# Kernel tuning notes

Measured on AMD Instinct MI355X. Metric: run time of the kernel, lower is better.

Reference implementation:

```python
import jax, jax.numpy as jnp
import numpy as np

N_NODES = 100000


def gcn_conv(x, W, b, src, dst, n):
    """PyG GCNConv: add self-loops, symmetric normalization, aggregate."""
    x = x @ W  # [N, out]
    loop = jnp.arange(n, dtype=src.dtype)
    src_f = jnp.concatenate([src, loop])  # sources (message origins)
    dst_f = jnp.concatenate([dst, loop])  # targets (aggregation index)
    ones = jnp.ones(src_f.shape[0], dtype=x.dtype)
    deg = jax.ops.segment_sum(ones, dst_f, num_segments=n)
    dinv = jnp.where(deg > 0, jax.lax.rsqrt(deg), 0.0)
    norm = dinv[src_f] * dinv[dst_f]  # [E+N]
    msg = x[src_f] * norm[:, None]  # gather + scale
    out = jax.ops.segment_sum(msg, dst_f, num_segments=n)  # scatter-add
    return out + b


def setup_inputs() -> dict:
    key = jax.random.key(0)
    k1, k2, k3, k4 = jax.random.split(key, 4)
    in_f, hid, ncls = 128, 128, 64
    n_edges = 1600000
    x = jax.random.normal(k1, (N_NODES, in_f), dtype=jnp.float32)
    W1 = jax.random.normal(k2, (in_f, hid), dtype=jnp.float32) * (1.0 / np.sqrt(in_f))
    b1 = jnp.zeros((hid,), dtype=jnp.float32)
    W2 = jax.random.normal(k3, (hid, ncls), dtype=jnp.float32) * (1.0 / np.sqrt(hid))
    b2 = jnp.zeros((ncls,), dtype=jnp.float32)
    edge_index = jax.random.randint(k4, (2, n_edges), 0, N_NODES, dtype=jnp.int32)
    return {"x": x, "W1": W1, "b1": b1, "W2": W2, "b2": b2, "edge_index": edge_index}


def reference(x, W1, b1, W2, b2, edge_index):
    src, dst = edge_index[0], edge_index[1]
    n = x.shape[0]
    h = gcn_conv(x, W1, b1, src, dst, n)
    h = jax.nn.relu(h)
    # dropout p=0.5 is identity in eval mode
    h = gcn_conv(h, W2, b2, src, dst, n)
    return jax.nn.log_softmax(h, axis=1)
```

## Files before the change

### kernel.cpp

```cpp
#include <hip/hip_runtime.h>
#include <math.h>

#define N_NODES 100000
#define N_EDGES 1600000
#define NB 391
#define MROWS 100096
#define CH 3200
#define ZROW N_NODES

typedef __attribute__((ext_vector_type(8))) short short8;
typedef __attribute__((ext_vector_type(4))) float f32x4;
typedef __attribute__((ext_vector_type(2))) float f32x2;

__device__ __forceinline__ short f2b(float f) {
    unsigned u = __float_as_uint(f);
    unsigned r = (u + 0x7FFFu + ((u >> 16) & 1u)) >> 16;
    return (short)r;
}
__device__ __forceinline__ unsigned pk2(float a, float b) {
    return (unsigned)(unsigned short)f2b(a) | ((unsigned)(unsigned short)f2b(b) << 16);
}
__device__ __forceinline__ unsigned char f2q(float v) {
    return (unsigned char)(__builtin_amdgcn_cvt_pk_fp8_f32(v, 0.f, 0, false) & 0xFF);
}
__device__ __forceinline__ void acc2(f32x2* a, unsigned u) {
    a[0] += __builtin_amdgcn_cvt_pk_f32_fp8((int)u, false);
    a[1] += __builtin_amdgcn_cvt_pk_f32_fp8((int)u, true);
}

__device__ __forceinline__ short8 pack8t(const float* __restrict__ p) {
    float4 v0 = ((const float4*)p)[0];
    float4 v1 = ((const float4*)p)[1];
    union { unsigned u[4]; short8 s; } r;
    r.u[0] = __builtin_amdgcn_perm(__float_as_uint(v0.y), __float_as_uint(v0.x), 0x07060302u);
    r.u[1] = __builtin_amdgcn_perm(__float_as_uint(v0.w), __float_as_uint(v0.z), 0x07060302u);
    r.u[2] = __builtin_amdgcn_perm(__float_as_uint(v1.y), __float_as_uint(v1.x), 0x07060302u);
    r.u[3] = __builtin_amdgcn_perm(__float_as_uint(v1.w), __float_as_uint(v1.z), 0x07060302u);
    return r.s;
}

__global__ __launch_bounds__(512) void init_misc(int* __restrict__ bcnt,
                                                 unsigned* __restrict__ y1s,
                                                 unsigned* __restrict__ y2s) {
    int t = threadIdx.x;
    if (t < NB) bcnt[t] = 0;
    if (t < 32) y1s[t] = 0;
    if (t < 16) y2s[t] = 0;
}

__global__ __launch_bounds__(256) void bucket_count(const int* __restrict__ dst,
                                                    int* __restrict__ bcnt) {
    __shared__ int h[NB];
    int t = threadIdx.x;
    for (int i = t; i < NB; i += 256) h[i] = 0;
    __syncthreads();
    for (int e = blockIdx.x * 256 + t; e < N_EDGES; e += gridDim.x * 256)
        atomicAdd(&h[dst[e] >> 8], 1);
    __syncthreads();
    for (int i = t; i < NB; i += 256)
        if (h[i]) atomicAdd(&bcnt[i], h[i]);
}

__global__ __launch_bounds__(512) void bucket_scan(const int* __restrict__ bcnt,
                                                   int* __restrict__ boffs,
                                                   int* __restrict__ bcur) {
    __shared__ int s[512];
    int t = threadIdx.x;
    int v = (t < NB) ? bcnt[t] : 0;
    s[t] = v;
    __syncthreads();
    for (int off = 1; off < 512; off <<= 1) {
        int u = (t >= off) ? s[t - off] : 0;
        __syncthreads();
        s[t] += u;
        __syncthreads();
    }
    if (t < NB) {
        int ex = s[t] - v;
        boffs[t] = ex;
        bcur[t] = ex;
    }
    if (t == 0) boffs[NB] = N_EDGES;
}

__global__ __launch_bounds__(256) void bucket_scatter(const int* __restrict__ src,
                                                      const int* __restrict__ dst,
                                                      int* __restrict__ bcur,
                                                      unsigned* __restrict__ pairs) {
    __shared__ unsigned lw[CH];
    __shared__ short lb[CH];
    __shared__ int cnt[NB];
    __shared__ int lstart[NB];
    int t = threadIdx.x;
    int e0 = blockIdx.x * CH;
    int n = min(CH, N_EDGES - e0);
    for (int i = t; i < NB; i += 256) cnt[i] = 0;
    __syncthreads();
    for (int i = t; i < n; i += 256) {
        int s = src[e0 + i], d = dst[e0 + i];
        lw[i] = ((unsigned)(d & 255) << 24) | (unsigned)s;
        int b = d >> 8;
        lb[i] = (short)b;
        atomicAdd(&cnt[b], 1);
    }
    __syncthreads();
    for (int b = t; b < NB; b += 256) {
        int c = cnt[b];
        lstart[b] = c ? atomicAdd(&bcur[b], c) : 0;
        cnt[b] = 0;
    }
    __syncthreads();
    for (int i = t; i < n; i += 256) {
        int b = lb[i];
        int lo = atomicAdd(&cnt[b], 1);
        pairs[lstart[b] + lo] = lw[i];
    }
}

__global__ __launch_bounds__(256) void csr_fill_bucket(const unsigned* __restrict__ pairs,
                                                       const int* __restrict__ boffs,
                                                       int2* __restrict__ rinfo,
                                                       float* __restrict__ dinv,
                                                       int* __restrict__ srcs) {
    __shared__ int lcnt[256];
    __shared__ int ls[256];
    int t = threadIdx.x, b = blockIdx.x, base = b << 8;
    lcnt[t] = 0;
    __syncthreads();
    int lo_e = boffs[b], hi_e = boffs[b + 1];
    for (int i = lo_e + t; i < hi_e; i += 256)
        atomicAdd(&lcnt[pairs[i] >> 24], 1);
    __syncthreads();
    int c = lcnt[t];
    int cpad = (c + 8) & ~7;
    ls[t] = cpad;
    __syncthreads();
    for (int off = 1; off < 256; off <<= 1) {
        int u = (t >= off) ? ls[t - off] : 0;
        __syncthreads();
        ls[t] += u;
        __syncthreads();
    }
    int pbase = ((lo_e + 7) & ~7) + b * 2056;
    int rp = pbase + ls[t] - cpad;
    int node = base + t;
    if (node < N_NODES) {
        rinfo[node] = make_int2(rp, rp + cpad);
        dinv[node] = rsqrtf((float)(c + 1));
        srcs[rp] = node;
    }
    __syncthreads();
    lcnt[t] = rp + 1;
    __syncthreads();
    for (int i = lo_e + t; i < hi_e; i += 256) {
        unsigned p = pairs[i];
        int li = p >> 24;
        int pos = atomicAdd(&lcnt[li], 1);
        srcs[pos] = (int)(p & 0xFFFFFFu);
    }
    __syncthreads();
    for (int i = lcnt[t], stop = rp + cpad; i < stop; ++i) srcs[i] = ZROW;
}

__global__ __launch_bounds__(256) void convert_w(const float* __restrict__ W1,
                                                 const float* __restrict__ W2,
                                                 short* __restrict__ w1h,
                                                 short* __restrict__ w2h) {
    int id = blockIdx.x * 256 + threadIdx.x;
    if (id < 128 * 128) {
        int n = id >> 7, k = id & 127;
        w1h[id] = f2b(W1[k * 128 + n]);
    } else if (id < 128 * 128 + 64 * 128) {
        int j = id - 128 * 128;
        int n = j >> 7, k = j & 127;
        w2h[j] = f2b(W2[k * 64 + n]);
    }
}

__global__ __launch_bounds__(512) void gemm1_mfma(const float* __restrict__ X,
                                                  const short* __restrict__ Wt,
                                                  const float* __restrict__ dinv,
                                                  unsigned char* __restrict__ Yf) {
    __shared__ short Ws[128 * 128];
    const int t = threadIdx.x;
    for (int i = t * 8; i < 128 * 128; i += 512 * 8)
        *(short8*)(Ws + i) = *(const short8*)(Wt + i);
    __syncthreads();

    const int w = t >> 6, lane = t & 63;
    const int m = lane & 15, q = lane >> 4;
    const int r0 = blockIdx.x * 128 + w * 16;
    const int ra = min(r0 + m, N_NODES - 1);

    f32x4 acc[8];
#pragma unroll
    for (int c = 0; c < 8; ++c) acc[c] = (f32x4)(0.f);

#pragma unroll
    for (int kk = 0; kk < 4; ++kk) {
        const int koff = kk * 32 + q * 8;
        short8 a = pack8t(X + (size_t)ra * 128 + koff);
#pragma unroll
        for (int c = 0; c < 8; ++c) {
            short8 bh = *(const short8*)(Ws + (c * 16 + m) * 128 + koff);
            acc[c] = __builtin_amdgcn_mfma_f32_16x16x32_bf16(a, bh, acc[c], 0, 0, 0);
        }
    }

    const int rb0 = r0 + q * 4;
    f32x4 dv = *(const f32x4*)(dinv + rb0);
#pragma unroll
    for (int c = 0; c < 8; ++c) {
        const int col = c * 16 + m;
#pragma unroll
        for (int r = 0; r < 4; ++r) {
            int row = rb0 + r;
            if (row < N_NODES) Yf[(size_t)row * 128 + col] = f2q(acc[c][r] * dv[r]);
        }
    }
}

__global__ __launch_bounds__(512) void gemm2_mfma(const short* __restrict__ H,
                                                  const short* __restrict__ Wt,
                                                  const float* __restrict__ dinv,
                                                  unsigned char* __restrict__ Yf) {
    __shared__ short Ws[64 * 128];
    const int t = threadIdx.x;
    for (int i = t * 8; i < 64 * 128; i += 512 * 8)
        *(short8*)(Ws + i) = *(const short8*)(Wt + i);
    __syncthreads();

    const int w = t >> 6, lane = t & 63;
    const int m = lane & 15, q = lane >> 4;
    const int r0 = blockIdx.x * 128 + w * 16;

    f32x4 acc[4];
#pragma unroll
    for (int c = 0; c < 4; ++c) acc[c] = (f32x4)(0.f);

#pragma unroll
    for (int kk = 0; kk < 4; ++kk) {
        const int koff = kk * 32 + q * 8;
        short8 a = *(const short8*)(H + (size_t)(r0 + m) * 128 + koff);
#pragma unroll
        for (int c = 0; c < 4; ++c) {
            short8 bh = *(const short8*)(Ws + (c * 16 + m) * 128 + koff);
            acc[c] = __builtin_amdgcn_mfma_f32_16x16x32_bf16(a, bh, acc[c], 0, 0, 0);
        }
    }

    const int rb0 = r0 + q * 4;
    f32x4 dv = *(const f32x4*)(dinv + rb0);
#pragma unroll
    for (int c = 0; c < 4; ++c) {
        const int col = c * 16 + m;
#pragma unroll
        for (int r = 0; r < 4; ++r) {
            int row = rb0 + r;
            if (row < N_NODES) Yf[(size_t)row * 64 + col] = f2q(acc[c][r] * dv[r]);
        }
    }
}

__global__ __launch_bounds__(256) void agg_relu(const int2* __restrict__ rinfo,
                                                const int* __restrict__ srcs,
                                                const unsigned char* __restrict__ Yf,
                                                const float* __restrict__ dinv,
                                                const float* __restrict__ b,
                                                short* __restrict__ Hb) {
    int t = threadIdx.x;
    int lane = t & 63, w = t >> 6;
    int half = lane >> 5, li = lane & 31;
    int d0 = blockIdx.x * 8 + 2 * w;
    int d1 = d0 + 1;
    const unsigned fo = (unsigned)(li << 2);
    int2 r0 = rinfo[d0], r1 = rinfo[d1];
    f32x2 a0[2] = {(f32x2)(0.f), (f32x2)(0.f)};
    f32x2 a1[2] = {(f32x2)(0.f), (f32x2)(0.f)};
    int e0 = r0.x, n0 = r0.y, e1 = r1.x, n1 = r1.y;
    uint4 s0 = *(const uint4*)(srcs + e0 + 4 * half);
    uint4 s1 = *(const uint4*)(srcs + e1 + 4 * half);
    bool c0 = true, c1 = true;
    for (;;) {
        bool p0 = c0, p1 = c1;
        unsigned g00, g01, g02, g03, g10, g11, g12, g13;
        if (p0) {
            g00 = *(const unsigned*)(Yf + (((unsigned)s0.x << 7) + fo));
            g01 = *(const unsigned*)(Yf + (((unsigned)s0.y << 7) + fo));
            g02 = *(const unsigned*)(Yf + (((unsigned)s0.z << 7) + fo));
            g03 = *(const unsigned*)(Yf + (((unsigned)s0.w << 7) + fo));
            e0 += 8;
            c0 = e0 < n0;
        }
        if (p1) {
            g10 = *(const unsigned*)(Yf + (((unsigned)s1.x << 7) + fo));
            g11 = *(const unsigned*)(Yf + (((unsigned)s1.y << 7) + fo));
            g12 = *(const unsigned*)(Yf + (((unsigned)s1.z << 7) + fo));
            g13 = *(const unsigned*)(Yf + (((unsigned)s1.w << 7) + fo));
            e1 += 8;
            c1 = e1 < n1;
        }
        if (c0) s0 = *(const uint4*)(srcs + e0 + 4 * half);
        if (c1) s1 = *(const uint4*)(srcs + e1 + 4 * half);
        if (p0) { acc2(a0, g00); acc2(a0, g01); acc2(a0, g02); acc2(a0, g03); }
        if (p1) { acc2(a1, g10); acc2(a1, g11); acc2(a1, g12); acc2(a1, g13); }
        if (!(c0 | c1)) break;
    }
    float t00 = a0[0][0], t01 = a0[0][1], t02 = a0[1][0], t03 = a0[1][1];
    float t10 = a1[0][0], t11 = a1[0][1], t12 = a1[1][0], t13 = a1[1][1];
    t00 += __shfl_xor(t00, 32); t01 += __shfl_xor(t01, 32);
    t02 += __shfl_xor(t02, 32); t03 += __shfl_xor(t03, 32);
    t10 += __shfl_xor(t10, 32); t11 += __shfl_xor(t11, 32);
    t12 += __shfl_xor(t12, 32); t13 += __shfl_xor(t13, 32);
    int dd = half ? d1 : d0;
    float s0f = half ? t10 : t00;
    float s1f = half ? t11 : t01;
    float s2f = half ? t12 : t02;
    float s3f = half ? t13 : t03;
    float sc = dinv[dd];
    float4 bb = ((const float4*)b)[li];
    float v0 = fmaxf(sc * s0f + bb.x, 0.f);
    float v1 = fmaxf(sc * s1f + bb.y, 0.f);
    float v2 = fmaxf(sc * s2f + bb.z, 0.f);
    float v3 = fmaxf(sc * s3f + bb.w, 0.f);
    ((uint2*)Hb)[(size_t)dd * 32 + li] = make_uint2(pk2(v0, v1), pk2(v2, v3));
}

__global__ __launch_bounds__(256) void agg_lsm(const int2* __restrict__ rinfo,
                                               const int* __restrict__ srcs,
                                               const unsigned char* __restrict__ Yf,
                                               const float* __restrict__ dinv,
                                               const float* __restrict__ b,
                                               float* __restrict__ out) {
    int t = threadIdx.x;
    int lane = t & 63, w = t >> 6;
    int gi = lane >> 4, li = lane & 15;
    int d0 = blockIdx.x * 8 + 2 * w;
    int d1 = d0 + 1;
    const unsigned fo = (unsigned)(li << 2);
    int2 r0 = rinfo[d0], r1 = rinfo[d1];
    f32x2 a0[2] = {(f32x2)(0.f), (f32x2)(0.f)};
    f32x2 a1[2] = {(f32x2)(0.f), (f32x2)(0.f)};
    int e0 = r0.x, n0 = r0.y, e1 = r1.x, n1 = r1.y;
    uint2 s0 = *(const uint2*)(srcs + e0 + 2 * gi);
    uint2 s1 = *(const uint2*)(srcs + e1 + 2 * gi);
    bool c0 = true, c1 = true;
    for (;;) {
        bool p0 = c0, p1 = c1;
        unsigned g00, g01, g10, g11;
        if (p0) {
            g00 = *(const unsigned*)(Yf + (((unsigned)s0.x << 6) + fo));
            g01 = *(const unsigned*)(Yf + (((unsigned)s0.y << 6) + fo));
            e0 += 8;
            c0 = e0 < n0;
        }
        if (p1) {
            g10 = *(const unsigned*)(Yf + (((unsigned)s1.x << 6) + fo));
            g11 = *(const unsigned*)(Yf + (((unsigned)s1.y << 6) + fo));
            e1 += 8;
            c1 = e1 < n1;
        }
        if (c0) s0 = *(const uint2*)(srcs + e0 + 2 * gi);
        if (c1) s1 = *(const uint2*)(srcs + e1 + 2 * gi);
        if (p0) { acc2(a0, g00); acc2(a0, g01); }
        if (p1) { acc2(a1, g10); acc2(a1, g11); }
        if (!(c0 | c1)) break;
    }
    float t00 = a0[0][0], t01 = a0[0][1], t02 = a0[1][0], t03 = a0[1][1];
    float t10 = a1[0][0], t11 = a1[0][1], t12 = a1[1][0], t13 = a1[1][1];
    t00 += __shfl_xor(t00, 16); t00 += __shfl_xor(t00, 32);
    t01 += __shfl_xor(t01, 16); t01 += __shfl_xor(t01, 32);
    t02 += __shfl_xor(t02, 16); t02 += __shfl_xor(t02, 32);
    t03 += __shfl_xor(t03, 16); t03 += __shfl_xor(t03, 32);
    t10 += __shfl_xor(t10, 16); t10 += __shfl_xor(t10, 32);
    t11 += __shfl_xor(t11, 16); t11 += __shfl_xor(t11, 32);
    t12 += __shfl_xor(t12, 16); t12 += __shfl_xor(t12, 32);
    t13 += __shfl_xor(t13, 16); t13 += __shfl_xor(t13, 32);
    int gsel = gi >> 1;
    int dd = gsel ? d1 : d0;
    float s0f = gsel ? t10 : t00;
    float s1f = gsel ? t11 : t01;
    float s2f = gsel ? t12 : t02;
    float s3f = gsel ? t13 : t03;
    float sc = dinv[dd];
    float4 bb = ((const float4*)b)[li];
    float v0 = sc * s0f + bb.x;
    float v1 = sc * s1f + bb.y;
    float v2 = sc * s2f + bb.z;
    float v3 = sc * s3f + bb.w;
    float m = fmaxf(fmaxf(v0, v1), fmaxf(v2, v3));
#pragma unroll
    for (int o = 1; o <= 8; o <<= 1) m = fmaxf(m, __shfl_xor(m, o));
    float su = __expf(v0 - m) + __expf(v1 - m) + __expf(v2 - m) + __expf(v3 - m);
#pragma unroll
    for (int o = 1; o <= 8; o <<= 1) su += __shfl_xor(su, o);
    float ls = m + logf(su);
    if ((gi & 1) == 0)
        ((float4*)out)[(size_t)dd * 16 + li] =
            make_float4(v0 - ls, v1 - ls, v2 - ls, v3 - ls);
}

extern "C" void kernel_launch(void* const* d_in, const int* in_sizes, int n_in,
                              void* d_out, int out_size, void* d_ws, size_t ws_size,
                              hipStream_t stream) {
    const float* x  = (const float*)d_in[0];
    const float* W1 = (const float*)d_in[1];
    const float* b1 = (const float*)d_in[2];
    const float* W2 = (const float*)d_in[3];
    const float* b2 = (const float*)d_in[4];
    const int* edge = (const int*)d_in[5];
    const int* src = edge;
    const int* dst = edge + N_EDGES;
    float* out = (float*)d_out;

    char* ws = (char*)d_ws;
    int*           bcnt  = (int*)(ws + 0);
    int*           boffs = (int*)(ws + 2048);
    int*           bcur  = (int*)(ws + 4096);
    float*         dinv  = (float*)(ws + 6144);
    int2*          rinfo = (int2*)(ws + 406528);
    int*           srcs  = (int*)(ws + 1206528);
    unsigned*      pairs = (unsigned*)(ws + 14012672);
    short*         w1h   = (short*)(ws + 20412672);
    short*         w2h   = (short*)(ws + 20445440);
    unsigned char* y1f   = (unsigned char*)(ws + 20461824);
    short*         h1b   = (short*)(ws + 33274112);
    unsigned char* y2f   = (unsigned char*)(ws + 58898688);

    init_misc<<<1, 512, 0, stream>>>(bcnt,
                                     (unsigned*)(y1f + (size_t)N_NODES * 128),
                                     (unsigned*)(y2f + (size_t)N_NODES * 64));

    bucket_count<<<512, 256, 0, stream>>>(dst, bcnt);
    bucket_scan<<<1, 512, 0, stream>>>(bcnt, boffs, bcur);
    bucket_scatter<<<(N_EDGES + CH - 1) / CH, 256, 0, stream>>>(src, dst, bcur, pairs);
    csr_fill_bucket<<<NB, 256, 0, stream>>>(pairs, boffs, rinfo, dinv, srcs);

    convert_w<<<(128 * 128 + 64 * 128 + 255) / 256, 256, 0, stream>>>(W1, W2, w1h, w2h);

    gemm1_mfma<<<MROWS / 128, 512, 0, stream>>>(x, w1h, dinv, y1f);
    agg_relu<<<N_NODES / 8, 256, 0, stream>>>(rinfo, srcs, y1f, dinv, b1, h1b);

    gemm2_mfma<<<MROWS / 128, 512, 0, stream>>>(h1b, w2h, dinv, y2f);
    agg_lsm<<<N_NODES / 8, 256, 0, stream>>>(rinfo, srcs, y2f, dinv, b2, out);
}
```

Measured before the change: 262.8 us.

## Remap aggregation kernels to small lane groups per node with 16-byte gathers

Both aggregation kernels now give each destination node a small group of lanes: 8 lanes with 16 features each for layer 1, 4 lanes for layer 2. Each lane gathers 16-byte fp8 rows and software-pipelines the source-index and feature loads two steps ahead. This removes the cross-half shuffle reductions and uses wider loads, so each wave handles 8 or 16 nodes instead of 2. In exchange, each wave loops up to its longest node's degree, and the shorter nodes pad with loads from the zero row, which can waste bandwidth when degrees vary.

```diff
diff --git a/kernel.cpp b/kernel.cpp
--- a/kernel.cpp
+++ b/kernel.cpp
@@ -26,6 +26,9 @@
 __device__ __forceinline__ void acc2(f32x2* a, unsigned u) {
     a[0] += __builtin_amdgcn_cvt_pk_f32_fp8((int)u, false);
     a[1] += __builtin_amdgcn_cvt_pk_f32_fp8((int)u, true);
+}
+__device__ __forceinline__ void acc16(f32x2* a, uint4 u) {
+    acc2(a + 0, u.x); acc2(a + 2, u.y); acc2(a + 4, u.z); acc2(a + 6, u.w);
 }
 
 __device__ __forceinline__ short8 pack8t(const float* __restrict__ p) {
@@ -270,60 +273,52 @@
                                                 short* __restrict__ Hb) {
     int t = threadIdx.x;
     int lane = t & 63, w = t >> 6;
-    int half = lane >> 5, li = lane & 31;
-    int d0 = blockIdx.x * 8 + 2 * w;
-    int d1 = d0 + 1;
-    const unsigned fo = (unsigned)(li << 2);
-    int2 r0 = rinfo[d0], r1 = rinfo[d1];
-    f32x2 a0[2] = {(f32x2)(0.f), (f32x2)(0.f)};
-    f32x2 a1[2] = {(f32x2)(0.f), (f32x2)(0.f)};
-    int e0 = r0.x, n0 = r0.y, e1 = r1.x, n1 = r1.y;
-    uint4 s0 = *(const uint4*)(srcs + e0 + 4 * half);
-    uint4 s1 = *(const uint4*)(srcs + e1 + 4 * half);
-    bool c0 = true, c1 = true;
-    for (;;) {
-        bool p0 = c0, p1 = c1;
-        unsigned g00, g01, g02, g03, g10, g11, g12, g13;
-        if (p0) {
-            g00 = *(const unsigned*)(Yf + (((unsigned)s0.x << 7) + fo));
-            g01 = *(const unsigned*)(Yf + (((unsigned)s0.y << 7) + fo));
-            g02 = *(const unsigned*)(Yf + (((unsigned)s0.z << 7) + fo));
-            g03 = *(const unsigned*)(Yf + (((unsigned)s0.w << 7) + fo));
-            e0 += 8;
-            c0 = e0 < n0;
-        }
-        if (p1) {
-            g10 = *(const unsigned*)(Yf + (((unsigned)s1.x << 7) + fo));
-            g11 = *(const unsigned*)(Yf + (((unsigned)s1.y << 7) + fo));
-            g12 = *(const unsigned*)(Yf + (((unsigned)s1.z << 7) + fo));
-            g13 = *(const unsigned*)(Yf + (((unsigned)s1.w << 7) + fo));
-            e1 += 8;
-            c1 = e1 < n1;
-        }
-        if (c0) s0 = *(const uint4*)(srcs + e0 + 4 * half);
-        if (c1) s1 = *(const uint4*)(srcs + e1 + 4 * half);
-        if (p0) { acc2(a0, g00); acc2(a0, g01); acc2(a0, g02); acc2(a0, g03); }
-        if (p1) { acc2(a1, g10); acc2(a1, g11); acc2(a1, g12); acc2(a1, g13); }
-        if (!(c0 | c1)) break;
-    }
-    float t00 = a0[0][0], t01 = a0[0][1], t02 = a0[1][0], t03 = a0[1][1];
-    float t10 = a1[0][0], t11 = a1[0][1], t12 = a1[1][0], t13 = a1[1][1];
-    t00 += __shfl_xor(t00, 32); t01 += __shfl_xor(t01, 32);
-    t02 += __shfl_xor(t02, 32); t03 += __shfl_xor(t03, 32);
-    t10 += __shfl_xor(t10, 32); t11 += __shfl_xor(t11, 32);
-    t12 += __shfl_xor(t12, 32); t13 += __shfl_xor(t13, 32);
-    int dd = half ? d1 : d0;
-    float s0f = half ? t10 : t00;
-    float s1f = half ? t11 : t01;
-    float s2f = half ? t12 : t02;
-    float s3f = half ? t13 : t03;
-    float sc = dinv[dd];
-    float4 bb = ((const float4*)b)[li];
-    float v0 = fmaxf(sc * s0f + bb.x, 0.f);
-    float v1 = fmaxf(sc * s1f + bb.y, 0.f);
-    float v2 = fmaxf(sc * s2f + bb.z, 0.f);
-    float v3 = fmaxf(sc * s3f + bb.w, 0.f);
-    ((uint2*)Hb)[(size_t)dd * 32 + li] = make_uint2(pk2(v0, v1), pk2(v2, v3));
+    int g = lane >> 3, fl = lane & 7;
+    int node = blockIdx.x * 32 + w * 8 + g;
+    const unsigned fo = (unsigned)(fl << 4);
+    int2 r = rinfo[node];
+    int e = r.x, len = r.y - r.x;
+    int mx = len;
+    mx = max(mx, __shfl_xor(mx, 8));
+    mx = max(mx, __shfl_xor(mx, 16));
+    mx = max(mx, __shfl_xor(mx, 32));
+    f32x2 a[8];
+#pragma unroll
+    for (int i = 0; i < 8; ++i) a[i] = (f32x2)(0.f);
+
+    auto lsrc = [&](int i) -> unsigned {
+        int s = srcs[e + min(i, len - 1)];
+        return (i < len) ? (unsigned)s : (unsigned)ZROW;
+    };
+    unsigned sA0 = lsrc(0), sA1 = lsrc(1);
+    uint4 GA0 = *(const uint4*)(Yf + ((sA0 << 7) + fo));
+    uint4 GA1 = *(const uint4*)(Yf + ((sA1 << 7) + fo));
+    unsigned sB0 = lsrc(2), sB1 = lsrc(3);
+    for (int i = 0; i < mx; i += 2) {
+        uint4 GB0 = *(const uint4*)(Yf + ((sB0 << 7) + fo));
+        uint4 GB1 = *(const uint4*)(Yf + ((sB1 << 7) + fo));
+        unsigned sC0 = lsrc(i + 4), sC1 = lsrc(i + 5);
+        acc16(a, GA0); acc16(a, GA1);
+        GA0 = GB0; GA1 = GB1; sB0 = sC0; sB1 = sC1;
+    }
+
+    float sc = dinv[node];
+    const float4* bf = (const float4*)b;
+    float bb[16];
+    *(float4*)(bb + 0)  = bf[fl * 4 + 0];
+    *(float4*)(bb + 4)  = bf[fl * 4 + 1];
+    *(float4*)(bb + 8)  = bf[fl * 4 + 2];
+    *(float4*)(bb + 12) = bf[fl * 4 + 3];
+    unsigned u[8];
+#pragma unroll
+    for (int k = 0; k < 8; ++k) {
+        float v0 = fmaxf(sc * a[k][0] + bb[2 * k], 0.f);
+        float v1 = fmaxf(sc * a[k][1] + bb[2 * k + 1], 0.f);
+        u[k] = pk2(v0, v1);
+    }
+    uint4* hp = (uint4*)Hb + (size_t)node * 16 + fl * 2;
+    hp[0] = make_uint4(u[0], u[1], u[2], u[3]);
+    hp[1] = make_uint4(u[4], u[5], u[6], u[7]);
 }
 
 __global__ __launch_bounds__(256) void agg_lsm(const int2* __restrict__ rinfo,
@@ -334,70 +329,65 @@
                                                float* __restrict__ out) {
     int t = threadIdx.x;
     int lane = t & 63, w = t >> 6;
-    int gi = lane >> 4, li = lane & 15;
-    int d0 = blockIdx.x * 8 + 2 * w;
-    int d1 = d0 + 1;
-    const unsigned fo = (unsigned)(li << 2);
-    int2 r0 = rinfo[d0], r1 = rinfo[d1];
-    f32x2 a0[2] = {(f32x2)(0.f), (f32x2)(0.f)};
-    f32x2 a1[2] = {(f32x2)(0.f), (f32x2)(0.f)};
-    int e0 = r0.x, n0 = r0.y, e1 = r1.x, n1 = r1.y;
-    uint2 s0 = *(const uint2*)(srcs + e0 + 2 * gi);
-    uint2 s1 = *(const uint2*)(srcs + e1 + 2 * gi);
-    bool c0 = true, c1 = true;
-    for (;;) {
-        bool p0 = c0, p1 = c1;
-        unsigned g00, g01, g10, g11;
-        if (p0) {
-            g00 = *(const unsigned*)(Yf + (((unsigned)s0.x << 6) + fo));
-            g01 = *(const unsigned*)(Yf + (((unsigned)s0.y << 6) + fo));
-            e0 += 8;
-            c0 = e0 < n0;
-        }
-        if (p1) {
-            g10 = *(const unsigned*)(Yf + (((unsigned)s1.x << 6) + fo));
-            g11 = *(const unsigned*)(Yf + (((unsigned)s1.y << 6) + fo));
-            e1 += 8;
-            c1 = e1 < n1;
-        }
-        if (c0) s0 = *(const uint2*)(srcs + e0 + 2 * gi);
-        if (c1) s1 = *(const uint2*)(srcs + e1 + 2 * gi);
-        if (p0) { acc2(a0, g00); acc2(a0, g01); }
-        if (p1) { acc2(a1, g10); acc2(a1, g11); }
-        if (!(c0 | c1)) break;
-    }
-    float t00 = a0[0][0], t01 = a0[0][1], t02 = a0[1][0], t03 = a0[1][1];
-    float t10 = a1[0][0], t11 = a1[0][1], t12 = a1[1][0], t13 = a1[1][1];
-    t00 += __shfl_xor(t00, 16); t00 += __shfl_xor(t00, 32);
-    t01 += __shfl_xor(t01, 16); t01 += __shfl_xor(t01, 32);
-    t02 += __shfl_xor(t02, 16); t02 += __shfl_xor(t02, 32);
-    t03 += __shfl_xor(t03, 16); t03 += __shfl_xor(t03, 32);
-    t10 += __shfl_xor(t10, 16); t10 += __shfl_xor(t10, 32);
-    t11 += __shfl_xor(t11, 16); t11 += __shfl_xor(t11, 32);
-    t12 += __shfl_xor(t12, 16); t12 += __shfl_xor(t12, 32);
-    t13 += __shfl_xor(t13, 16); t13 += __shfl_xor(t13, 32);
-    int gsel = gi >> 1;
-    int dd = gsel ? d1 : d0;
-    float s0f = gsel ? t10 : t00;
-    float s1f = gsel ? t11 : t01;
-    float s2f = gsel ? t12 : t02;
-    float s3f = gsel ? t13 : t03;
-    float sc = dinv[dd];
-    float4 bb = ((const float4*)b)[li];
-    float v0 = sc * s0f + bb.x;
-    float v1 = sc * s1f + bb.y;
-    float v2 = sc * s2f + bb.z;
-    float v3 = sc * s3f + bb.w;
-    float m = fmaxf(fmaxf(v0, v1), fmaxf(v2, v3));
-#pragma unroll
-    for (int o = 1; o <= 8; o <<= 1) m = fmaxf(m, __shfl_xor(m, o));
-    float su = __expf(v0 - m) + __expf(v1 - m) + __expf(v2 - m) + __expf(v3 - m);
-#pragma unroll
-    for (int o = 1; o <= 8; o <<= 1) su += __shfl_xor(su, o);
+    int g = lane >> 2, fl = lane & 3;
+    int node = blockIdx.x * 64 + w * 16 + g;
+    int nd = min(node, N_NODES - 1);
+    const unsigned fo = (unsigned)(fl << 4);
+    int2 r = rinfo[nd];
+    int e = r.x, len = r.y - r.x;
+    int mx = len;
+    mx = max(mx, __shfl_xor(mx, 4));
+    mx = max(mx, __shfl_xor(mx, 8));
+    mx = max(mx, __shfl_xor(mx, 16));
+    mx = max(mx, __shfl_xor(mx, 32));
+    f32x2 a[8];
+#pragma unroll
+    for (int i = 0; i < 8; ++i) a[i] = (f32x2)(0.f);
+
+    auto lsrc = [&](int i) -> unsigned {
+        int s = srcs[e + min(i, len - 1)];
+        return (i < len) ? (unsigned)s : (unsigned)ZROW;
+    };
+    unsigned sA0 = lsrc(0), sA1 = lsrc(1);
+    uint4 GA0 = *(const uint4*)(Yf + ((sA0 << 6) + fo));
+    uint4 GA1 = *(const uint4*)(Yf + ((sA1 << 6) + fo));
+    unsigned sB0 = lsrc(2), sB1 = lsrc(3);
+    for (int i = 0; i < mx; i += 2) {
+        uint4 GB0 = *(const uint4*)(Yf + ((sB0 << 6) + fo));
+        uint4 GB1 = *(const uint4*)(Yf + ((sB1 << 6) + fo));
+        unsigned sC0 = lsrc(i + 4), sC1 = lsrc(i + 5);
+        acc16(a, GA0); acc16(a, GA1);
+        GA0 = GB0; GA1 = GB1; sB0 = sC0; sB1 = sC1;
+    }
+
+    float sc = dinv[nd];
+    const float4* bf = (const float4*)b;
+    float bb[16];
+    *(float4*)(bb + 0)  = bf[fl * 4 + 0];
+    *(float4*)(bb + 4)  = bf[fl * 4 + 1];
+    *(float4*)(bb + 8)  = bf[fl * 4 + 2];
+    *(float4*)(bb + 12) = bf[fl * 4 + 3];
+    float v[16];
+#pragma unroll
+    for (int j = 0; j < 16; ++j) v[j] = sc * a[j >> 1][j & 1] + bb[j];
+    float m = v[0];
+#pragma unroll
+    for (int j = 1; j < 16; ++j) m = fmaxf(m, v[j]);
+    m = fmaxf(m, __shfl_xor(m, 1));
+    m = fmaxf(m, __shfl_xor(m, 2));
+    float su = 0.f;
+#pragma unroll
+    for (int j = 0; j < 16; ++j) su += __expf(v[j] - m);
+    su += __shfl_xor(su, 1);
+    su += __shfl_xor(su, 2);
     float ls = m + logf(su);
-    if ((gi & 1) == 0)
-        ((float4*)out)[(size_t)dd * 16 + li] =
-            make_float4(v0 - ls, v1 - ls, v2 - ls, v3 - ls);
+    if (node < N_NODES) {
+        float4* op = (float4*)out + (size_t)node * 16 + fl * 4;
+        op[0] = make_float4(v[0] - ls,  v[1] - ls,  v[2] - ls,  v[3] - ls);
+        op[1] = make_float4(v[4] - ls,  v[5] - ls,  v[6] - ls,  v[7] - ls);
+        op[2] = make_float4(v[8] - ls,  v[9] - ls,  v[10] - ls, v[11] - ls);
+        op[3] = make_float4(v[12] - ls, v[13] - ls, v[14] - ls, v[15] - ls);
+    }
 }
 
 extern "C" void kernel_launch(void* const* d_in, const int* in_sizes, int n_in,
@@ -439,8 +429,8 @@
     convert_w<<<(128 * 128 + 64 * 128 + 255) / 256, 256, 0, stream>>>(W1, W2, w1h, w2h);
 
     gemm1_mfma<<<MROWS / 128, 512, 0, stream>>>(x, w1h, dinv, y1f);
-    agg_relu<<<N_NODES / 8, 256, 0, stream>>>(rinfo, srcs, y1f, dinv, b1, h1b);
+    agg_relu<<<N_NODES / 32, 256, 0, stream>>>(rinfo, srcs, y1f, dinv, b1, h1b);
 
     gemm2_mfma<<<MROWS / 128, 512, 0, stream>>>(h1b, w2h, dinv, y2f);
-    agg_lsm<<<N_NODES / 8, 256, 0, stream>>>(rinfo, srcs, y2f, dinv, b2, out);
-}
+    agg_lsm<<<(N_NODES + 63) / 64, 256, 0, stream>>>(rinfo, srcs, y2f, dinv, b2, out);
+}
```

Result: no change. 260.6 us (-0.8%).
